# Performance work log

Measured on AMD Instinct MI355X. Metric: run time of the kernel, lower is better.

The kernel has to match this reference:

```python
import jax, jax.numpy as jnp
import numpy as np

ENC_LEN, B, ENC2, DEC, E = 1024, 64, 1024, 512, 512

def setup_inputs() -> dict:
    key = jax.random.key(0)
    k1, k2, k3, k4 = jax.random.split(key, 4)
    enc_output = jax.random.normal(k1, (ENC_LEN, B, ENC2), dtype=jnp.float32)
    s = jax.random.normal(k2, (1, B, DEC), dtype=jnp.float32)
    # torch Linear weights: [out_features, in_features], no bias
    W_attn = jax.random.normal(k3, (E, ENC2 + DEC), dtype=jnp.float32) * (1.0 / np.sqrt(ENC2 + DEC))
    W_v = jax.random.normal(k4, (1, E), dtype=jnp.float32) * (1.0 / np.sqrt(E))
    return {"enc_output": enc_output, "s": s, "W_attn": W_attn, "W_v": W_v}

def reference(enc_output, s, W_attn, W_v):
    # cat([enc_output, s.repeat(L,1,1)], -1) @ W_attn.T  ==  enc @ Wa_e.T + s @ Wa_s.T (broadcast)
    enc2 = enc_output.shape[-1]
    Wa_e = W_attn[:, :enc2]          # [E, 2*enc_hid]
    Wa_s = W_attn[:, enc2:]          # [E, dec_hid]
    pre = jnp.einsum('lbc,ec->lbe', enc_output, Wa_e) + jnp.einsum('obd,ed->obe', s, Wa_s)
    engry = jnp.tanh(pre)            # [L, B, E]
    attention = jnp.einsum('lbe,oe->lbo', engry, W_v)[..., 0].T  # [B, L]
    return jax.nn.softmax(attention, axis=-1)
```

## Files before the change

### kernel.cpp

```cpp
#include <hip/hip_runtime.h>
#include <hip/hip_bf16.h>
#include <stdint.h>

typedef __bf16 bf16;
typedef __bf16 bf16x4 __attribute__((ext_vector_type(4)));
typedef __bf16 bf16x8 __attribute__((ext_vector_type(8)));
typedef float  f32x4  __attribute__((ext_vector_type(4)));

#define L_TOT 1024
#define B_TOT 64
#define C_TOT 1024
#define D_TOT 512
#define E_TOT 512
#define M_TOT (L_TOT * B_TOT)
#define W_LD  (C_TOT + D_TOT)

#define BM 64
#define BN 512
#define BK 32
#define NT 512
#define NKT (C_TOT / BK)

__device__ __forceinline__ void gload_lds16(const void* g, void* l) {
  __builtin_amdgcn_global_load_lds(
      (const __attribute__((address_space(1))) unsigned int*)(uintptr_t)g,
      (__attribute__((address_space(3))) unsigned int*)(uintptr_t)l,
      16, 0, 0);
}

__device__ __forceinline__ bf16x4 cvt4(float4 v) {
  bf16x4 o;
  o[0] = (bf16)v.x; o[1] = (bf16)v.y; o[2] = (bf16)v.z; o[3] = (bf16)v.w;
  return o;
}

__global__ void convert_we_kernel(const float* __restrict__ Wattn,
                                  bf16* __restrict__ Wb) {
  const int e = blockIdx.x;
  const int t = threadIdx.x;
  const float4 v = ((const float4*)(Wattn + (size_t)e * W_LD))[t];
  ((bf16x4*)(Wb + (size_t)e * C_TOT))[t] = cvt4(v);
}

__global__ void sb_kernel(const float* __restrict__ s,
                          const float* __restrict__ Wattn,
                          float* __restrict__ sb) {
  const int e = blockIdx.x;
  const int b = threadIdx.x;
  const float4* sr = (const float4*)(s + (size_t)b * D_TOT);
  const float4* wr = (const float4*)(Wattn + (size_t)e * W_LD + C_TOT);
  float acc = 0.f;
#pragma unroll 4
  for (int i = 0; i < D_TOT / 4; ++i) {
    float4 a = sr[i], w = wr[i];
    acc += a.x * w.x; acc += a.y * w.y; acc += a.z * w.z; acc += a.w * w.w;
  }
  sb[(size_t)b * E_TOT + e] = acc;
}

__global__ __launch_bounds__(NT, 4)
void gemm_tanh_dot_kernel(const float* __restrict__ A,
                          const bf16*  __restrict__ Wb,
                          const float* __restrict__ sb,
                          const float* __restrict__ Wv,
                          float* __restrict__ logits) {
  __shared__ __align__(16) char smem[2 * 4096 + 2 * 32768];
  char* const As0 = smem;
  char* const As1 = smem + 4096;
  char* const Bs0 = smem + 8192;
  char* const Bs1 = smem + 8192 + 32768;

  const int tid  = threadIdx.x;
  const int lane = tid & 63;
  const int wn   = tid >> 6;
  const int fr   = lane & 15;
  const int fg   = lane >> 4;
  const int m0   = blockIdx.x * BM;

  const int a_row = tid >> 3;
  const int a_k4  = (tid & 7) << 2;
  const float* gA = A + (size_t)(m0 + a_row) * C_TOT + a_k4;
  const int a_s   = ((a_row & 1) << 2) | (a_k4 >> 3);
  const int aw_off = ((a_row >> 1) << 7)
                   + ((a_s ^ ((a_row >> 1) & 7)) << 4)
                   + ((a_k4 & 4) << 1);

  const int b_s = (tid & 7) ^ ((tid >> 3) & 7);
  const int b_e = ((tid >> 3) << 1) + (b_s >> 2);
  const bf16* bsrc = Wb + (size_t)b_e * C_TOT + ((b_s & 3) << 3);
  const int b_dst = tid << 4;

  const int xo = ((((fr & 1) << 2) | fg) ^ ((fr >> 1) & 7)) << 4;
  const int ro = ((fr >> 1) << 7) + xo;

  f32x4 acc[4][4];
#pragma unroll
  for (int i = 0; i < 4; ++i)
#pragma unroll
    for (int j = 0; j < 4; ++j)
      acc[i][j] = (f32x4){0.f, 0.f, 0.f, 0.f};

  float4 avA = *(const float4*)(gA);
#pragma unroll
  for (int i = 0; i < 4; ++i)
    gload_lds16(bsrc + i * 131072, Bs0 + b_dst + i * 8192);
  *(bf16x4*)(As0 + aw_off) = cvt4(avA);
  avA = *(const float4*)(gA + BK);
  __syncthreads();

  char* Ac = As0; char* An = As1; char* Bc = Bs0; char* Bn = Bs1;
#pragma unroll 1
  for (int kt = 0; kt < NKT; ++kt) {
    if (kt + 1 < NKT) {
      const int k1 = (kt + 1) * BK;
#pragma unroll
      for (int i = 0; i < 4; ++i)
        gload_lds16(bsrc + k1 + i * 131072, Bn + b_dst + i * 8192);
      *(bf16x4*)(An + aw_off) = cvt4(avA);
      const int k2 = (kt + 2 < NKT) ? (kt + 2) * BK : 0;
      avA = *(const float4*)(gA + k2);
    }
    bf16x8 af[4], bfr[4];
#pragma unroll
    for (int am = 0; am < 4; ++am)
      af[am] = *(const bf16x8*)(Ac + am * 1024 + ro);
#pragma unroll
    for (int bn = 0; bn < 4; ++bn)
      bfr[bn] = *(const bf16x8*)(Bc + (wn << 12) + bn * 1024 + ro);
#pragma unroll
    for (int am = 0; am < 4; ++am)
#pragma unroll
      for (int bn = 0; bn < 4; ++bn)
        acc[am][bn] = __builtin_amdgcn_mfma_f32_16x16x32_bf16(
            af[am], bfr[bn], acc[am][bn], 0, 0, 0);
    __syncthreads();
    char* t0 = Ac; Ac = An; An = t0;
    char* t1 = Bc; Bc = Bn; Bn = t1;
  }

  float wv[4];
#pragma unroll
  for (int bn = 0; bn < 4; ++bn)
    wv[bn] = Wv[(wn << 6) + (bn << 4) + fr];

  float* red = (float*)smem;
#pragma unroll
  for (int am = 0; am < 4; ++am) {
#pragma unroll
    for (int j = 0; j < 4; ++j) {
      const int mloc = (am << 4) + (fg << 2) + j;
      const float* sbr = sb + (size_t)mloc * E_TOT + (wn << 6) + fr;
      float c = 0.f;
#pragma unroll
      for (int bn = 0; bn < 4; ++bn)
        c += tanhf(acc[am][bn][j] + sbr[bn << 4]) * wv[bn];
      c += __shfl_xor(c, 1, 64);
      c += __shfl_xor(c, 2, 64);
      c += __shfl_xor(c, 4, 64);
      c += __shfl_xor(c, 8, 64);
      if (fr == 0) red[(wn << 6) + mloc] = c;
    }
  }
  __syncthreads();
  if (tid < BM) {
    float v = 0.f;
#pragma unroll
    for (int w = 0; w < 8; ++w) v += red[(w << 6) + tid];
    logits[m0 + tid] = v;
  }
}

__global__ __launch_bounds__(256)
void softmax_kernel(const float* __restrict__ logits, float* __restrict__ out) {
  const int b = blockIdx.x;
  const int t = threadIdx.x;
  const int lane = t & 63, w = t >> 6;
  __shared__ float sm[8];
  float x[4];
  float mx = -3.4e38f;
#pragma unroll
  for (int i = 0; i < 4; ++i) {
    const int l = t + (i << 8);
    x[i] = logits[(size_t)l * 64 + b];
    mx = fmaxf(mx, x[i]);
  }
#pragma unroll
  for (int off = 1; off < 64; off <<= 1)
    mx = fmaxf(mx, __shfl_xor(mx, off, 64));
  if (lane == 0) sm[w] = mx;
  __syncthreads();
  mx = fmaxf(fmaxf(sm[0], sm[1]), fmaxf(sm[2], sm[3]));
  float ex[4], ssum = 0.f;
#pragma unroll
  for (int i = 0; i < 4; ++i) { ex[i] = expf(x[i] - mx); ssum += ex[i]; }
#pragma unroll
  for (int off = 1; off < 64; off <<= 1)
    ssum += __shfl_xor(ssum, off, 64);
  if (lane == 0) sm[4 + w] = ssum;
  __syncthreads();
  const float inv = 1.0f / (sm[4] + sm[5] + sm[6] + sm[7]);
#pragma unroll
  for (int i = 0; i < 4; ++i)
    out[(size_t)b * 1024 + t + (i << 8)] = ex[i] * inv;
}

extern "C" void kernel_launch(void* const* d_in, const int* in_sizes, int n_in,
                              void* d_out, int out_size, void* d_ws, size_t ws_size,
                              hipStream_t stream) {
  const float* enc = (const float*)d_in[0];
  const float* s   = (const float*)d_in[1];
  const float* Wat = (const float*)d_in[2];
  const float* Wv  = (const float*)d_in[3];
  float* out = (float*)d_out;

  char* ws = (char*)d_ws;
  bf16*  Wb     = (bf16*)ws;
  float* sb     = (float*)(ws + (1u << 20));
  float* logits = (float*)(ws + (1u << 20) + (128u << 10));

  convert_we_kernel<<<E_TOT, 256, 0, stream>>>(Wat, Wb);
  sb_kernel<<<E_TOT, 64, 0, stream>>>(s, Wat, sb);
  gemm_tanh_dot_kernel<<<M_TOT / BM, NT, 0, stream>>>(enc, Wb, sb, Wv, logits);
  softmax_kernel<<<B_TOT, 256, 0, stream>>>(logits, out);
}
```

Baseline: 178.6 us.

## Hand-schedule GEMM main loop with inline-asm loads and explicit waitcnt barriers

Rewrites the double-buffered K loop as a two-stage unrolled pipeline. A-tile loads are issued through inline asm global_load_dwordx4, and explicit s_waitcnt vmcnt/lgkmcnt counts plus raw s_barrier replace __syncthreads. This lets the next tile's loads stay in flight while the MFMAs run, instead of draining at every barrier. It relies on hand-counted outstanding load totals, which is fragile: a miscount could race on LDS or read stale data.

```diff
diff --git a/kernel.cpp b/kernel.cpp
--- a/kernel.cpp
+++ b/kernel.cpp
@@ -28,9 +28,9 @@
       16, 0, 0);
 }
 
-__device__ __forceinline__ bf16x4 cvt4(float4 v) {
+__device__ __forceinline__ bf16x4 cvt4(f32x4 v) {
   bf16x4 o;
-  o[0] = (bf16)v.x; o[1] = (bf16)v.y; o[2] = (bf16)v.z; o[3] = (bf16)v.w;
+  o[0] = (bf16)v[0]; o[1] = (bf16)v[1]; o[2] = (bf16)v[2]; o[3] = (bf16)v[3];
   return o;
 }
 
@@ -39,7 +39,9 @@
   const int e = blockIdx.x;
   const int t = threadIdx.x;
   const float4 v = ((const float4*)(Wattn + (size_t)e * W_LD))[t];
-  ((bf16x4*)(Wb + (size_t)e * C_TOT))[t] = cvt4(v);
+  bf16x4 o;
+  o[0] = (bf16)v.x; o[1] = (bf16)v.y; o[2] = (bf16)v.z; o[3] = (bf16)v.w;
+  ((bf16x4*)(Wb + (size_t)e * C_TOT))[t] = o;
 }
 
 __global__ void sb_kernel(const float* __restrict__ s,
@@ -100,26 +102,12 @@
     for (int j = 0; j < 4; ++j)
       acc[i][j] = (f32x4){0.f, 0.f, 0.f, 0.f};
 
-  float4 avA = *(const float4*)(gA);
-#pragma unroll
-  for (int i = 0; i < 4; ++i)
-    gload_lds16(bsrc + i * 131072, Bs0 + b_dst + i * 8192);
-  *(bf16x4*)(As0 + aw_off) = cvt4(avA);
-  avA = *(const float4*)(gA + BK);
-  __syncthreads();
-
-  char* Ac = As0; char* An = As1; char* Bc = Bs0; char* Bn = Bs1;
-#pragma unroll 1
-  for (int kt = 0; kt < NKT; ++kt) {
-    if (kt + 1 < NKT) {
-      const int k1 = (kt + 1) * BK;
-#pragma unroll
-      for (int i = 0; i < 4; ++i)
-        gload_lds16(bsrc + k1 + i * 131072, Bn + b_dst + i * 8192);
-      *(bf16x4*)(An + aw_off) = cvt4(avA);
-      const int k2 = (kt + 2 < NKT) ? (kt + 2) * BK : 0;
-      avA = *(const float4*)(gA + k2);
-    }
+  auto stageB = [&](char* Bbuf, int kc) {
+#pragma unroll
+    for (int i = 0; i < 4; ++i)
+      gload_lds16(bsrc + kc + i * 131072, Bbuf + b_dst + i * 8192);
+  };
+  auto compute = [&](const char* Ac, const char* Bc) {
     bf16x8 af[4], bfr[4];
 #pragma unroll
     for (int am = 0; am < 4; ++am)
@@ -133,10 +121,56 @@
       for (int bn = 0; bn < 4; ++bn)
         acc[am][bn] = __builtin_amdgcn_mfma_f32_16x16x32_bf16(
             af[am], bfr[bn], acc[am][bn], 0, 0, 0);
-    __syncthreads();
-    char* t0 = Ac; Ac = An; An = t0;
-    char* t1 = Bc; Bc = Bn; Bn = t1;
-  }
+  };
+
+  f32x4 av_p, av_q, av0;
+
+  asm volatile("global_load_dwordx4 %0, %1, off"
+               : "=v"(av0) : "v"(gA) : "memory");
+  stageB(Bs0, 0);
+  asm volatile("s_waitcnt vmcnt(4)" ::: "memory");
+  __builtin_amdgcn_sched_barrier(0);
+  *(bf16x4*)(As0 + aw_off) = cvt4(av0);
+  {
+    const float* ap = gA + BK;
+    asm volatile("global_load_dwordx4 %0, %1, off"
+                 : "=v"(av_p) : "v"(ap) : "memory");
+  }
+
+#pragma unroll 1
+  for (int kp = 0; kp < 16; ++kp) {
+    const int t0 = kp << 1;
+    asm volatile("s_waitcnt vmcnt(1) lgkmcnt(0)" ::: "memory");
+    __builtin_amdgcn_s_barrier();
+    {
+      stageB(Bs1, (t0 + 1) * BK);
+      const float* ap = gA + ((t0 + 2) & 31) * BK;
+      asm volatile("global_load_dwordx4 %0, %1, off"
+                   : "=v"(av_q) : "v"(ap) : "memory");
+    }
+    compute(As0, Bs0);
+    asm volatile("s_waitcnt vmcnt(5)" ::: "memory");
+    __builtin_amdgcn_sched_barrier(0);
+    *(bf16x4*)(As1 + aw_off) = cvt4(av_p);
+    asm volatile("s_waitcnt vmcnt(1) lgkmcnt(0)" ::: "memory");
+    __builtin_amdgcn_s_barrier();
+    if (kp < 15) {
+      stageB(Bs0, (t0 + 2) * BK);
+      const float* ap = gA + ((t0 + 3) & 31) * BK;
+      asm volatile("global_load_dwordx4 %0, %1, off"
+                   : "=v"(av_p) : "v"(ap) : "memory");
+    }
+    compute(As1, Bs1);
+    if (kp < 15) {
+      asm volatile("s_waitcnt vmcnt(5)" ::: "memory");
+      __builtin_amdgcn_sched_barrier(0);
+      *(bf16x4*)(As0 + aw_off) = cvt4(av_q);
+    }
+  }
+
+  asm volatile("s_waitcnt vmcnt(0)" ::: "memory");
+  __builtin_amdgcn_sched_barrier(0);
+  asm volatile("" :: "v"(av_q));
 
   float wv[4];
 #pragma unroll
```

Result: faster. 171.3 us (-4.1%).

## Enlarge GEMM tile, stream fp32 A via direct-to-LDS loads, triple-buffer

Applied to the files above, without the earlier changes.

Doubles the M tile to 128 rows and switches to a 2x4 wave layout, so each wave holds a 4x8 grid of MFMA accumulators and the weight tile is reused across twice as many rows. The fp32 encoder tile is now copied straight into LDS with global_load_lds and converted to bf16 when fragments are read, instead of going through registers. A three-stage LDS ring with explicit vmcnt waits and barriers replaces the double buffer, to keep more loads in flight. The cost is about 144KB of LDS per block, which allows only one block (8 waves) per CU. It also doubles the fp32 A bytes held in LDS and adds conversion work in the inner loop.

```diff
diff --git a/kernel.cpp b/kernel.cpp
--- a/kernel.cpp
+++ b/kernel.cpp
@@ -15,7 +15,7 @@
 #define M_TOT (L_TOT * B_TOT)
 #define W_LD  (C_TOT + D_TOT)
 
-#define BM 64
+#define BM 128
 #define BN 512
 #define BK 32
 #define NT 512
@@ -28,18 +28,14 @@
       16, 0, 0);
 }
 
-__device__ __forceinline__ bf16x4 cvt4(float4 v) {
-  bf16x4 o;
-  o[0] = (bf16)v.x; o[1] = (bf16)v.y; o[2] = (bf16)v.z; o[3] = (bf16)v.w;
-  return o;
-}
-
 __global__ void convert_we_kernel(const float* __restrict__ Wattn,
                                   bf16* __restrict__ Wb) {
   const int e = blockIdx.x;
   const int t = threadIdx.x;
   const float4 v = ((const float4*)(Wattn + (size_t)e * W_LD))[t];
-  ((bf16x4*)(Wb + (size_t)e * C_TOT))[t] = cvt4(v);
+  bf16x4 o;
+  o[0] = (bf16)v.x; o[1] = (bf16)v.y; o[2] = (bf16)v.z; o[3] = (bf16)v.w;
+  ((bf16x4*)(Wb + (size_t)e * C_TOT))[t] = o;
 }
 
 __global__ void sb_kernel(const float* __restrict__ s,
@@ -58,114 +54,133 @@
   sb[(size_t)b * E_TOT + e] = acc;
 }
 
-__global__ __launch_bounds__(NT, 4)
+__global__ __launch_bounds__(NT, 2)
 void gemm_tanh_dot_kernel(const float* __restrict__ A,
                           const bf16*  __restrict__ Wb,
                           const float* __restrict__ sb,
                           const float* __restrict__ Wv,
                           float* __restrict__ logits) {
-  __shared__ __align__(16) char smem[2 * 4096 + 2 * 32768];
+  __shared__ __align__(16) char smem[3 * 16384 + 3 * 32768];
   char* const As0 = smem;
-  char* const As1 = smem + 4096;
-  char* const Bs0 = smem + 8192;
-  char* const Bs1 = smem + 8192 + 32768;
+  char* const As1 = smem + 16384;
+  char* const As2 = smem + 32768;
+  char* const Bs0 = smem + 49152;
+  char* const Bs1 = smem + 49152 + 32768;
+  char* const Bs2 = smem + 49152 + 65536;
 
   const int tid  = threadIdx.x;
   const int lane = tid & 63;
-  const int wn   = tid >> 6;
+  const int wid  = tid >> 6;
+  const int wm   = wid >> 2;
+  const int wn   = wid & 3;
   const int fr   = lane & 15;
   const int fg   = lane >> 4;
   const int m0   = blockIdx.x * BM;
 
   const int a_row = tid >> 3;
-  const int a_k4  = (tid & 7) << 2;
-  const float* gA = A + (size_t)(m0 + a_row) * C_TOT + a_k4;
-  const int a_s   = ((a_row & 1) << 2) | (a_k4 >> 3);
-  const int aw_off = ((a_row >> 1) << 7)
-                   + ((a_s ^ ((a_row >> 1) & 7)) << 4)
-                   + ((a_k4 & 4) << 1);
+  const int a_sg  = (tid & 7) ^ (a_row & 7);
+  const float* asrc = A + (size_t)(m0 + a_row) * C_TOT + (a_sg << 2);
+  const int a_dst = tid << 4;
 
   const int b_s = (tid & 7) ^ ((tid >> 3) & 7);
   const int b_e = ((tid >> 3) << 1) + (b_s >> 2);
   const bf16* bsrc = Wb + (size_t)b_e * C_TOT + ((b_s & 3) << 3);
   const int b_dst = tid << 4;
 
-  const int xo = ((((fr & 1) << 2) | fg) ^ ((fr >> 1) & 7)) << 4;
-  const int ro = ((fr >> 1) << 7) + xo;
-
-  f32x4 acc[4][4];
+  const int aoff = (wm << 13) + (fr << 7) + ((((fg << 1) ^ (fr & 7))) << 4);
+  const int boff = (wn << 13) + ((fr >> 1) << 7)
+                 + (((((fr & 1) << 2) | fg) ^ ((fr >> 1) & 7)) << 4);
+
+  f32x4 acc[4][8];
 #pragma unroll
   for (int i = 0; i < 4; ++i)
 #pragma unroll
-    for (int j = 0; j < 4; ++j)
+    for (int j = 0; j < 8; ++j)
       acc[i][j] = (f32x4){0.f, 0.f, 0.f, 0.f};
 
-  float4 avA = *(const float4*)(gA);
-#pragma unroll
-  for (int i = 0; i < 4; ++i)
-    gload_lds16(bsrc + i * 131072, Bs0 + b_dst + i * 8192);
-  *(bf16x4*)(As0 + aw_off) = cvt4(avA);
-  avA = *(const float4*)(gA + BK);
-  __syncthreads();
-
-  char* Ac = As0; char* An = As1; char* Bc = Bs0; char* Bn = Bs1;
-#pragma unroll 1
-  for (int kt = 0; kt < NKT; ++kt) {
-    if (kt + 1 < NKT) {
-      const int k1 = (kt + 1) * BK;
-#pragma unroll
-      for (int i = 0; i < 4; ++i)
-        gload_lds16(bsrc + k1 + i * 131072, Bn + b_dst + i * 8192);
-      *(bf16x4*)(An + aw_off) = cvt4(avA);
-      const int k2 = (kt + 2 < NKT) ? (kt + 2) * BK : 0;
-      avA = *(const float4*)(gA + k2);
+  auto stage = [&](char* Ai, char* Bi, int t) {
+    const int kcA = t << 5;
+    gload_lds16(asrc + kcA, Ai + a_dst);
+    gload_lds16(asrc + kcA + 65536, Ai + a_dst + 8192);
+    const int kcB = t << 5;
+#pragma unroll
+    for (int i = 0; i < 4; ++i)
+      gload_lds16(bsrc + kcB + i * 131072, Bi + b_dst + i * 8192);
+  };
+
+  auto compute = [&](const char* Ac, const char* Bc) {
+    bf16x8 af[4];
+#pragma unroll
+    for (int am = 0; am < 4; ++am) {
+      const int o = aoff + am * 2048;
+      f32x4 lo = *(const f32x4*)(Ac + o);
+      f32x4 hi = *(const f32x4*)(Ac + (o ^ 16));
+      bf16x8 f;
+      f[0] = (bf16)lo[0]; f[1] = (bf16)lo[1]; f[2] = (bf16)lo[2]; f[3] = (bf16)lo[3];
+      f[4] = (bf16)hi[0]; f[5] = (bf16)hi[1]; f[6] = (bf16)hi[2]; f[7] = (bf16)hi[3];
+      af[am] = f;
     }
-    bf16x8 af[4], bfr[4];
+    bf16x8 bfr[8];
+#pragma unroll
+    for (int bn = 0; bn < 8; ++bn)
+      bfr[bn] = *(const bf16x8*)(Bc + boff + bn * 1024);
 #pragma unroll
     for (int am = 0; am < 4; ++am)
-      af[am] = *(const bf16x8*)(Ac + am * 1024 + ro);
-#pragma unroll
-    for (int bn = 0; bn < 4; ++bn)
-      bfr[bn] = *(const bf16x8*)(Bc + (wn << 12) + bn * 1024 + ro);
-#pragma unroll
-    for (int am = 0; am < 4; ++am)
-#pragma unroll
-      for (int bn = 0; bn < 4; ++bn)
+#pragma unroll
+      for (int bn = 0; bn < 8; ++bn)
         acc[am][bn] = __builtin_amdgcn_mfma_f32_16x16x32_bf16(
             af[am], bfr[bn], acc[am][bn], 0, 0, 0);
-    __syncthreads();
-    char* t0 = Ac; Ac = An; An = t0;
-    char* t1 = Bc; Bc = Bn; Bn = t1;
-  }
-
-  float wv[4];
-#pragma unroll
-  for (int bn = 0; bn < 4; ++bn)
-    wv[bn] = Wv[(wn << 6) + (bn << 4) + fr];
+  };
+
+#define TILE(Ac, Bc, Ai, Bi, T, DO_ISSUE, WCNT)                         \
+  asm volatile("s_waitcnt vmcnt(" #WCNT ")" ::: "memory");              \
+  __builtin_amdgcn_sched_barrier(0);                                    \
+  __builtin_amdgcn_s_barrier();                                         \
+  __builtin_amdgcn_sched_barrier(0);                                    \
+  if (DO_ISSUE) stage(Ai, Bi, (T) + 2);                                 \
+  compute(Ac, Bc);
+
+  stage(As0, Bs0, 0);
+  stage(As1, Bs1, 1);
+
+#pragma unroll 1
+  for (int kp = 0; kp < 10; ++kp) {
+    const int t0 = kp * 3;
+    TILE(As0, Bs0, As2, Bs2, t0 + 0, true, 6);
+    TILE(As1, Bs1, As0, Bs0, t0 + 1, true, 6);
+    TILE(As2, Bs2, As1, Bs1, t0 + 2, true, 6);
+  }
+  TILE(As0, Bs0, As0, Bs0, 30, false, 6);
+  TILE(As1, Bs1, As1, Bs1, 31, false, 0);
+#undef TILE
+
+  float wv[8];
+#pragma unroll
+  for (int bn = 0; bn < 8; ++bn)
+    wv[bn] = Wv[(wn << 7) + (bn << 4) + fr];
 
   float* red = (float*)smem;
 #pragma unroll
   for (int am = 0; am < 4; ++am) {
 #pragma unroll
     for (int j = 0; j < 4; ++j) {
-      const int mloc = (am << 4) + (fg << 2) + j;
-      const float* sbr = sb + (size_t)mloc * E_TOT + (wn << 6) + fr;
+      const int mloc = (wm << 6) + (am << 4) + (fg << 2) + j;
+      const int b = mloc & 63;
+      const float* sbr = sb + (size_t)b * E_TOT + (wn << 7) + fr;
       float c = 0.f;
 #pragma unroll
-      for (int bn = 0; bn < 4; ++bn)
+      for (int bn = 0; bn < 8; ++bn)
         c += tanhf(acc[am][bn][j] + sbr[bn << 4]) * wv[bn];
       c += __shfl_xor(c, 1, 64);
       c += __shfl_xor(c, 2, 64);
       c += __shfl_xor(c, 4, 64);
       c += __shfl_xor(c, 8, 64);
-      if (fr == 0) red[(wn << 6) + mloc] = c;
+      if (fr == 0) red[(wn << 7) + mloc] = c;
     }
   }
   __syncthreads();
   if (tid < BM) {
-    float v = 0.f;
-#pragma unroll
-    for (int w = 0; w < 8; ++w) v += red[(w << 6) + tid];
+    float v = red[tid] + red[128 + tid] + red[256 + tid] + red[384 + tid];
     logits[m0 + tid] = v;
   }
 }
```

After: 160.9 us. -9.9%, faster.

## Retile GEMM to 128x256 with split-E halves, triple-buffered B and fast tanh

Applied to the files above, without the earlier changes.

The fused GEMM+tanh+dot kernel moves from 64x512 tiles to 128x256 tiles with BK=64. The E dimension is split across two blocks that write partial logits, and the softmax sums them. B tiles are triple-buffered through direct global-to-LDS loads, and A is prefetched with inline asm loads, explicit vmcnt waits, sched barriers and raised priority around the MFMA bursts. A block-index swizzle pairs the E halves for L2 reuse of A, and tanhf/expf are replaced with fast exp-based approximations. The aim is fewer barriers per K step, better overlap of memory and MFMA work, and a cheaper epilogue. The cost is reading enc twice (once per E half) and a larger LDS footprint with lower occupancy.

```diff
diff --git a/kernel.cpp b/kernel.cpp
--- a/kernel.cpp
+++ b/kernel.cpp
@@ -15,9 +15,9 @@
 #define M_TOT (L_TOT * B_TOT)
 #define W_LD  (C_TOT + D_TOT)
 
-#define BM 64
-#define BN 512
-#define BK 32
+#define BM 128
+#define BN 256
+#define BK 64
 #define NT 512
 #define NKT (C_TOT / BK)
 
@@ -28,10 +28,16 @@
       16, 0, 0);
 }
 
-__device__ __forceinline__ bf16x4 cvt4(float4 v) {
-  bf16x4 o;
-  o[0] = (bf16)v.x; o[1] = (bf16)v.y; o[2] = (bf16)v.z; o[3] = (bf16)v.w;
+__device__ __forceinline__ bf16x8 cvt8(f32x4 a, f32x4 b) {
+  bf16x8 o;
+  o[0]=(bf16)a[0]; o[1]=(bf16)a[1]; o[2]=(bf16)a[2]; o[3]=(bf16)a[3];
+  o[4]=(bf16)b[0]; o[5]=(bf16)b[1]; o[6]=(bf16)b[2]; o[7]=(bf16)b[3];
   return o;
+}
+
+__device__ __forceinline__ float tanh_fast(float x) {
+  float e = __expf(2.0f * x);
+  return 1.0f - __fdividef(2.0f, e + 1.0f);
 }
 
 __global__ void convert_we_kernel(const float* __restrict__ Wattn,
@@ -39,7 +45,9 @@
   const int e = blockIdx.x;
   const int t = threadIdx.x;
   const float4 v = ((const float4*)(Wattn + (size_t)e * W_LD))[t];
-  ((bf16x4*)(Wb + (size_t)e * C_TOT))[t] = cvt4(v);
+  bf16x4 o;
+  o[0]=(bf16)v.x; o[1]=(bf16)v.y; o[2]=(bf16)v.z; o[3]=(bf16)v.w;
+  ((bf16x4*)(Wb + (size_t)e * C_TOT))[t] = o;
 }
 
 __global__ void sb_kernel(const float* __restrict__ s,
@@ -58,40 +66,49 @@
   sb[(size_t)b * E_TOT + e] = acc;
 }
 
-__global__ __launch_bounds__(NT, 4)
+__global__ __launch_bounds__(NT, 2)
 void gemm_tanh_dot_kernel(const float* __restrict__ A,
                           const bf16*  __restrict__ Wb,
                           const float* __restrict__ sb,
                           const float* __restrict__ Wv,
-                          float* __restrict__ logits) {
-  __shared__ __align__(16) char smem[2 * 4096 + 2 * 32768];
-  char* const As0 = smem;
-  char* const As1 = smem + 4096;
-  char* const Bs0 = smem + 8192;
-  char* const Bs1 = smem + 8192 + 32768;
+                          float* __restrict__ logitsH) {
+  __shared__ __align__(16) char smem[2 * 16384 + 3 * 32768];
+  char* const Aa0 = smem;
+  char* const Aa1 = smem + 16384;
+  char* const Bq0 = smem + 32768;
+  char* const Bq1 = smem + 65536;
+  char* const Bq2 = smem + 98304;
 
   const int tid  = threadIdx.x;
   const int lane = tid & 63;
-  const int wn   = tid >> 6;
+  const int wid  = tid >> 6;
+  const int wm   = wid >> 2;
+  const int wn   = wid & 3;
   const int fr   = lane & 15;
   const int fg   = lane >> 4;
-  const int m0   = blockIdx.x * BM;
-
-  const int a_row = tid >> 3;
-  const int a_k4  = (tid & 7) << 2;
-  const float* gA = A + (size_t)(m0 + a_row) * C_TOT + a_k4;
-  const int a_s   = ((a_row & 1) << 2) | (a_k4 >> 3);
-  const int aw_off = ((a_row >> 1) << 7)
-                   + ((a_s ^ ((a_row >> 1) & 7)) << 4)
-                   + ((a_k4 & 4) << 1);
+
+  const int blk = blockIdx.x;
+  const int gx  = (blk & 7) | ((blk >> 4) << 3);
+  const int gy  = (blk >> 3) & 1;
+  const int m0  = gx << 7;
+  const int e0  = gy << 8;
+
+  const float* gA = A + (size_t)(m0 + (tid >> 2)) * C_TOT + ((tid & 3) << 4);
+  const int p_a  = tid >> 3;
+  const int rb_a = (tid >> 2) & 1;
+  const int hf_a = (tid >> 1) & 1;
+  const int qb_a = (tid & 1) << 1;
+  const int awo0 = hf_a * 8192 + p_a * 128 + ((((rb_a << 2) | qb_a))     ^ (p_a & 7)) * 16;
+  const int awo1 = hf_a * 8192 + p_a * 128 + ((((rb_a << 2) | (qb_a+1))) ^ (p_a & 7)) * 16;
 
   const int b_s = (tid & 7) ^ ((tid >> 3) & 7);
   const int b_e = ((tid >> 3) << 1) + (b_s >> 2);
-  const bf16* bsrc = Wb + (size_t)b_e * C_TOT + ((b_s & 3) << 3);
-  const int b_dst = tid << 4;
-
-  const int xo = ((((fr & 1) << 2) | fg) ^ ((fr >> 1) & 7)) << 4;
-  const int ro = ((fr >> 1) << 7) + xo;
+  const bf16* gB = Wb + (size_t)(e0 + b_e) * C_TOT + ((b_s & 3) << 3);
+  const int bdst = tid << 4;
+
+  const int sx  = (((((fr & 1) << 2) | fg)) ^ (fr >> 1)) << 4;
+  const int aro = ((wm << 5) + (fr >> 1)) * 128 + sx;
+  const int bro = ((wn << 5) + (fr >> 1)) * 128 + sx;
 
   f32x4 acc[4][4];
 #pragma unroll
@@ -100,78 +117,131 @@
     for (int j = 0; j < 4; ++j)
       acc[i][j] = (f32x4){0.f, 0.f, 0.f, 0.f};
 
-  float4 avA = *(const float4*)(gA);
-#pragma unroll
-  for (int i = 0; i < 4; ++i)
-    gload_lds16(bsrc + i * 131072, Bs0 + b_dst + i * 8192);
-  *(bf16x4*)(As0 + aw_off) = cvt4(avA);
-  avA = *(const float4*)(gA + BK);
-  __syncthreads();
-
-  char* Ac = As0; char* An = As1; char* Bc = Bs0; char* Bn = Bs1;
-#pragma unroll 1
-  for (int kt = 0; kt < NKT; ++kt) {
-    if (kt + 1 < NKT) {
-      const int k1 = (kt + 1) * BK;
-#pragma unroll
-      for (int i = 0; i < 4; ++i)
-        gload_lds16(bsrc + k1 + i * 131072, Bn + b_dst + i * 8192);
-      *(bf16x4*)(An + aw_off) = cvt4(avA);
-      const int k2 = (kt + 2 < NKT) ? (kt + 2) * BK : 0;
-      avA = *(const float4*)(gA + k2);
-    }
-    bf16x8 af[4], bfr[4];
-#pragma unroll
-    for (int am = 0; am < 4; ++am)
-      af[am] = *(const bf16x8*)(Ac + am * 1024 + ro);
-#pragma unroll
-    for (int bn = 0; bn < 4; ++bn)
-      bfr[bn] = *(const bf16x8*)(Bc + (wn << 12) + bn * 1024 + ro);
+  f32x4 av00, av01, av02, av03, av10, av11, av12, av13;
+
+  auto stageB = [&](char* Bp, int t) {
+    const bf16* sp = gB + (t << 6);
+    gload_lds16(sp,           Bp + bdst);
+    gload_lds16(sp + 131072,  Bp + bdst + 8192);
+    gload_lds16(sp + 32,          Bp + bdst + 16384);
+    gload_lds16(sp + 32 + 131072, Bp + bdst + 24576);
+  };
+
+#define LOADA(p, t)                                                            \
+  { const float* ap_ = gA + ((t) << 6);                                        \
+    asm volatile("global_load_dwordx4 %0, %1, off"           : "=v"(av##p##0) : "v"(ap_) : "memory"); \
+    asm volatile("global_load_dwordx4 %0, %1, off offset:16" : "=v"(av##p##1) : "v"(ap_) : "memory"); \
+    asm volatile("global_load_dwordx4 %0, %1, off offset:32" : "=v"(av##p##2) : "v"(ap_) : "memory"); \
+    asm volatile("global_load_dwordx4 %0, %1, off offset:48" : "=v"(av##p##3) : "v"(ap_) : "memory"); }
+
+#define WRITEA(Ap, p)                                                          \
+  { *(bf16x8*)((Ap) + awo0) = cvt8(av##p##0, av##p##1);                        \
+    *(bf16x8*)((Ap) + awo1) = cvt8(av##p##2, av##p##3); }
+
+  auto phase = [&](int kk, const char* Ap, const char* Bp) {
+    bf16x8 af[4], bf[4];
+    const char* Ab = Ap + kk * 8192  + aro;
+    const char* Bb = Bp + kk * 16384 + bro;
+#pragma unroll
+    for (int am = 0; am < 4; ++am) af[am] = *(const bf16x8*)(Ab + am * 1024);
+#pragma unroll
+    for (int bn = 0; bn < 4; ++bn) bf[bn] = *(const bf16x8*)(Bb + bn * 1024);
+    asm volatile("s_waitcnt lgkmcnt(0)" ::: "memory");
+    __builtin_amdgcn_sched_barrier(0);
+    __builtin_amdgcn_s_setprio(1);
 #pragma unroll
     for (int am = 0; am < 4; ++am)
 #pragma unroll
       for (int bn = 0; bn < 4; ++bn)
         acc[am][bn] = __builtin_amdgcn_mfma_f32_16x16x32_bf16(
-            af[am], bfr[bn], acc[am][bn], 0, 0, 0);
-    __syncthreads();
-    char* t0 = Ac; Ac = An; An = t0;
-    char* t1 = Bc; Bc = Bn; Bn = t1;
-  }
+            af[am], bf[bn], acc[am][bn], 0, 0, 0);
+    __builtin_amdgcn_s_setprio(0);
+    __builtin_amdgcn_sched_barrier(0);
+  };
+
+#define BARRIER()                                                              \
+  asm volatile("s_waitcnt lgkmcnt(0)" ::: "memory");                           \
+  __builtin_amdgcn_s_barrier();                                                \
+  __builtin_amdgcn_sched_barrier(0);
+
+  stageB(Bq0, 0);
+  LOADA(0, 0);
+  stageB(Bq1, 1);
+  LOADA(1, 1);
+  asm volatile("s_waitcnt vmcnt(8)" ::: "memory");
+  __builtin_amdgcn_sched_barrier(0);
+  WRITEA(Aa0, 0);
+  BARRIER();
+
+  char* B0 = Bq0; char* B1 = Bq1; char* B2 = Bq2;
+
+#pragma unroll 1
+  for (int kp = 0; kp < 7; ++kp) {
+    const int t = kp << 1;
+    stageB(B2, t + 2);
+    LOADA(0, t + 2);
+    asm volatile("s_waitcnt vmcnt(8)" ::: "memory");
+    __builtin_amdgcn_sched_barrier(0);
+    WRITEA(Aa1, 1);
+    phase(0, Aa0, B0);
+    phase(1, Aa0, B0);
+    BARRIER();
+    stageB(B0, t + 3);
+    LOADA(1, t + 3);
+    asm volatile("s_waitcnt vmcnt(8)" ::: "memory");
+    __builtin_amdgcn_sched_barrier(0);
+    WRITEA(Aa0, 0);
+    phase(0, Aa1, B1);
+    phase(1, Aa1, B1);
+    BARRIER();
+    char* tmp = B2; B2 = B1; B1 = B0; B0 = tmp;
+  }
+
+  asm volatile("s_waitcnt vmcnt(0)" ::: "memory");
+  __builtin_amdgcn_sched_barrier(0);
+  WRITEA(Aa1, 1);
+  phase(0, Aa0, B0);
+  phase(1, Aa0, B0);
+  BARRIER();
+  phase(0, Aa1, B1);
+  phase(1, Aa1, B1);
 
   float wv[4];
 #pragma unroll
   for (int bn = 0; bn < 4; ++bn)
-    wv[bn] = Wv[(wn << 6) + (bn << 4) + fr];
+    wv[bn] = Wv[e0 + (wn << 6) + (bn << 4) + fr];
 
   float* red = (float*)smem;
 #pragma unroll
   for (int am = 0; am < 4; ++am) {
 #pragma unroll
     for (int j = 0; j < 4; ++j) {
-      const int mloc = (am << 4) + (fg << 2) + j;
-      const float* sbr = sb + (size_t)mloc * E_TOT + (wn << 6) + fr;
+      const int mloc = (wm << 6) + (am << 4) + (fg << 2) + j;
+      const int bi = mloc & 63;
+      const float* sbr = sb + (size_t)bi * E_TOT + e0 + (wn << 6) + fr;
       float c = 0.f;
 #pragma unroll
       for (int bn = 0; bn < 4; ++bn)
-        c += tanhf(acc[am][bn][j] + sbr[bn << 4]) * wv[bn];
+        c += tanh_fast(acc[am][bn][j] + sbr[bn << 4]) * wv[bn];
       c += __shfl_xor(c, 1, 64);
       c += __shfl_xor(c, 2, 64);
       c += __shfl_xor(c, 4, 64);
       c += __shfl_xor(c, 8, 64);
-      if (fr == 0) red[(wn << 6) + mloc] = c;
+      if (fr == 0) red[(wn << 7) + mloc] = c;
     }
   }
   __syncthreads();
   if (tid < BM) {
-    float v = 0.f;
-#pragma unroll
-    for (int w = 0; w < 8; ++w) v += red[(w << 6) + tid];
-    logits[m0 + tid] = v;
-  }
+    float v = red[tid] + red[128 + tid] + red[256 + tid] + red[384 + tid];
+    logitsH[(size_t)gy * M_TOT + m0 + tid] = v;
+  }
+#undef LOADA
+#undef WRITEA
+#undef BARRIER
 }
 
 __global__ __launch_bounds__(256)
-void softmax_kernel(const float* __restrict__ logits, float* __restrict__ out) {
+void softmax_kernel(const float* __restrict__ lH, float* __restrict__ out) {
   const int b = blockIdx.x;
   const int t = threadIdx.x;
   const int lane = t & 63, w = t >> 6;
@@ -180,8 +250,8 @@
   float mx = -3.4e38f;
 #pragma unroll
   for (int i = 0; i < 4; ++i) {
-    const int l = t + (i << 8);
-    x[i] = logits[(size_t)l * 64 + b];
+    const int m = (t + (i << 8)) * 64 + b;
+    x[i] = lH[m] + lH[M_TOT + m];
     mx = fmaxf(mx, x[i]);
   }
 #pragma unroll
@@ -192,7 +262,7 @@
   mx = fmaxf(fmaxf(sm[0], sm[1]), fmaxf(sm[2], sm[3]));
   float ex[4], ssum = 0.f;
 #pragma unroll
-  for (int i = 0; i < 4; ++i) { ex[i] = expf(x[i] - mx); ssum += ex[i]; }
+  for (int i = 0; i < 4; ++i) { ex[i] = __expf(x[i] - mx); ssum += ex[i]; }
 #pragma unroll
   for (int off = 1; off < 64; off <<= 1)
     ssum += __shfl_xor(ssum, off, 64);
@@ -214,12 +284,12 @@
   float* out = (float*)d_out;
 
   char* ws = (char*)d_ws;
-  bf16*  Wb     = (bf16*)ws;
-  float* sb     = (float*)(ws + (1u << 20));
-  float* logits = (float*)(ws + (1u << 20) + (128u << 10));
+  bf16*  Wb      = (bf16*)ws;
+  float* sb      = (float*)(ws + (1u << 20));
+  float* logitsH = (float*)(ws + (1u << 20) + (128u << 10));
 
   convert_we_kernel<<<E_TOT, 256, 0, stream>>>(Wat, Wb);
   sb_kernel<<<E_TOT, 64, 0, stream>>>(s, Wat, sb);
-  gemm_tanh_dot_kernel<<<M_TOT / BM, NT, 0, stream>>>(enc, Wb, sb, Wv, logits);
-  softmax_kernel<<<B_TOT, 256, 0, stream>>>(logits, out);
-}
+  gemm_tanh_dot_kernel<<<(M_TOT / BM) * 2, NT, 0, stream>>>(enc, Wb, sb, Wv, logitsH);
+  softmax_kernel<<<B_TOT, 256, 0, stream>>>(logitsH, out);
+}
```

New measurement: 151.1 us (median of 2 runs). 1.18x faster.
